# Kernel optimization log

Measured on AMD Instinct MI355X. Metric: run time of the kernel, lower is better.

The kernel has to match this reference:

```python
import jax, jax.numpy as jnp
import numpy as np

N = 50000      # nodes
E = 800000     # edges (avg degree 16)
G = 128        # graphs in batch
IN = 128       # in_channels
H = 128        # hidden_dim
C = 10         # num_classes


def setup_inputs() -> dict:
    key = jax.random.key(0)
    ks = jax.random.split(key, 8)
    x = jax.random.normal(ks[0], (N, IN), dtype=jnp.float32)
    edge_index = jax.random.randint(ks[1], (2, E), 0, N)
    edge_attr = jax.random.uniform(ks[2], (E,), dtype=jnp.float32)
    batch = jnp.sort(jax.random.randint(ks[3], (N,), 0, G))
    def glorot(k, fan_in, fan_out):
        return jax.random.normal(k, (fan_in, fan_out), dtype=jnp.float32) / np.float32(np.sqrt(fan_in))
    return {
        "x": x,
        "edge_index": edge_index,
        "edge_attr": edge_attr,
        "batch": batch,
        "W1": glorot(ks[4], IN, H), "b1": jnp.zeros((H,), jnp.float32),
        "W2": glorot(ks[5], H, H), "b2": jnp.zeros((H,), jnp.float32),
        "W3": glorot(ks[6], H, C), "b3": jnp.zeros((C,), jnp.float32),
    }


def gcn_conv(x, src, dst, ew, W, b, n):
    # symmetric GCN normalization (self-loops already appended, weight 1)
    deg = jax.ops.segment_sum(ew, dst, num_segments=n)            # [N]
    dinv = jnp.where(deg > 0, jax.lax.rsqrt(deg), 0.0)
    norm = dinv[src] * ew * dinv[dst]                             # [E+N]
    h = x @ W                                                     # [N, out]
    agg = jax.ops.segment_sum(h[src] * norm[:, None], dst, num_segments=n)
    return agg + b


def reference(x, edge_index, edge_attr, batch, W1, b1, W2, b2, W3, b3):
    n = x.shape[0]
    loop = jnp.arange(n)
    src = jnp.concatenate([edge_index[0], loop])
    dst = jnp.concatenate([edge_index[1], loop])
    ew = jnp.concatenate([edge_attr, jnp.ones((n,), edge_attr.dtype)])
    h = jax.nn.relu(gcn_conv(x, src, dst, ew, W1, b1, n))   # dropout is identity in eval
    h = jax.nn.relu(gcn_conv(h, src, dst, ew, W2, b2, n))
    h = gcn_conv(h, src, dst, ew, W3, b3, n)                 # [N, C]
    # global mean pool over graphs
    sums = jax.ops.segment_sum(h, batch, num_segments=G)     # [G, C]
    cnt = jax.ops.segment_sum(jnp.ones((n,), h.dtype), batch, num_segments=G)
    pooled = sums / jnp.maximum(cnt, 1.0)[:, None]
    return jax.nn.log_softmax(pooled, axis=1)
```

## Files before the change

### kernel.cpp

```cpp
#include <hip/hip_runtime.h>

#define NN 50000
#define NE 800000
#define NG 128
#define DIM 128
#define CO 10
#define CAP 64

typedef unsigned long long ull;
typedef unsigned short ushort;

static __device__ __forceinline__ ushort f2bf(float f) {
    unsigned int u = __float_as_uint(f);
    unsigned int r = (u + 0x7FFF + ((u >> 16) & 1)) >> 16;
    return (ushort)r;
}

__global__ void k_ell(const int* __restrict__ src, const int* __restrict__ dst,
                      const float* __restrict__ ew, int* __restrict__ cnt,
                      ull* __restrict__ ell) {
    int e = blockIdx.x * blockDim.x + threadIdx.x;
    if (e >= NE) return;
    int d = dst[e], s = src[e];
    int slot = atomicAdd(&cnt[d], 1);
    if (slot < CAP) {
        ull rec = ((ull)__float_as_uint(ew[e]) << 32) | (unsigned int)s;
        ell[(size_t)d * CAP + slot] = rec;
    }
}

__global__ __launch_bounds__(256) void k_deg(const int* __restrict__ cnt,
                                             const ull* __restrict__ ell,
                                             float* __restrict__ dinv) {
    int node = blockIdx.x * 4 + (threadIdx.x >> 6);
    int lane = threadIdx.x & 63;
    if (node >= NN) return;
    int n = cnt[node];
    float w = 0.0f;
    if (lane < n) w = __uint_as_float((unsigned int)(ell[(size_t)node * CAP + lane] >> 32));
#pragma unroll
    for (int off = 32; off; off >>= 1) w += __shfl_down(w, off);
    if (lane == 0) dinv[node] = rsqrtf(1.0f + w);
}

__global__ __launch_bounds__(256) void k_scale(const int* __restrict__ cnt,
                                               ull* __restrict__ ell,
                                               const float* __restrict__ dinv) {
    int node = blockIdx.x * 4 + (threadIdx.x >> 6);
    int lane = threadIdx.x & 63;
    if (node >= NN) return;
    int n = cnt[node];
    if (lane >= n) return;
    size_t idx = (size_t)node * CAP + lane;
    ull rec = ell[idx];
    int s = (int)(unsigned int)(rec & 0xffffffffu);
    float ew = __uint_as_float((unsigned int)(rec >> 32));
    float v = dinv[node] * ew * dinv[s];
    ell[idx] = ((ull)__float_as_uint(v) << 32) | (unsigned int)s;
}

__global__ __launch_bounds__(256) void k_gemm128(const float* __restrict__ A,
                                                 const float* __restrict__ W,
                                                 ushort* __restrict__ C, int M) {
    __shared__ float As[64][33];
    __shared__ float Bs[32][132];
    int tid = threadIdx.x;
    int block_row = blockIdx.x * 64;
    int tx = tid & 15;
    int ty = tid >> 4;
    int r0 = ty * 4;
    int c1 = tx * 4, c2 = 64 + tx * 4;
    float acc[4][8];
#pragma unroll
    for (int i = 0; i < 4; i++)
#pragma unroll
        for (int j = 0; j < 8; j++) acc[i][j] = 0.0f;

    for (int k0 = 0; k0 < 128; k0 += 32) {
#pragma unroll
        for (int l = 0; l < 2; l++) {
            int idx = tid + l * 256;
            int ar = idx >> 3;
            int ac = (idx & 7) * 4;
            int grow = block_row + ar;
            if (grow >= M) grow = M - 1;
            float4 v = *(const float4*)&A[(size_t)grow * 128 + k0 + ac];
            As[ar][ac + 0] = v.x; As[ar][ac + 1] = v.y;
            As[ar][ac + 2] = v.z; As[ar][ac + 3] = v.w;
        }
#pragma unroll
        for (int l = 0; l < 4; l++) {
            int idx = tid + l * 256;
            int br = idx >> 5;
            int bc = (idx & 31) * 4;
            float4 v = *(const float4*)&W[(size_t)(k0 + br) * 128 + bc];
            *(float4*)&Bs[br][bc] = v;
        }
        __syncthreads();
#pragma unroll
        for (int kk = 0; kk < 32; kk++) {
            float a0 = As[r0 + 0][kk];
            float a1 = As[r0 + 1][kk];
            float a2 = As[r0 + 2][kk];
            float a3 = As[r0 + 3][kk];
            float4 bl = *(float4*)&Bs[kk][c1];
            float4 bh = *(float4*)&Bs[kk][c2];
            acc[0][0] += a0 * bl.x; acc[0][1] += a0 * bl.y; acc[0][2] += a0 * bl.z; acc[0][3] += a0 * bl.w;
            acc[0][4] += a0 * bh.x; acc[0][5] += a0 * bh.y; acc[0][6] += a0 * bh.z; acc[0][7] += a0 * bh.w;
            acc[1][0] += a1 * bl.x; acc[1][1] += a1 * bl.y; acc[1][2] += a1 * bl.z; acc[1][3] += a1 * bl.w;
            acc[1][4] += a1 * bh.x; acc[1][5] += a1 * bh.y; acc[1][6] += a1 * bh.z; acc[1][7] += a1 * bh.w;
            acc[2][0] += a2 * bl.x; acc[2][1] += a2 * bl.y; acc[2][2] += a2 * bl.z; acc[2][3] += a2 * bl.w;
            acc[2][4] += a2 * bh.x; acc[2][5] += a2 * bh.y; acc[2][6] += a2 * bh.z; acc[2][7] += a2 * bh.w;
            acc[3][0] += a3 * bl.x; acc[3][1] += a3 * bl.y; acc[3][2] += a3 * bl.z; acc[3][3] += a3 * bl.w;
            acc[3][4] += a3 * bh.x; acc[3][5] += a3 * bh.y; acc[3][6] += a3 * bh.z; acc[3][7] += a3 * bh.w;
        }
        __syncthreads();
    }
#pragma unroll
    for (int i = 0; i < 4; i++) {
        int grow = block_row + r0 + i;
        if (grow < M) {
            ushort4 u1, u2;
            u1.x = f2bf(acc[i][0]); u1.y = f2bf(acc[i][1]); u1.z = f2bf(acc[i][2]); u1.w = f2bf(acc[i][3]);
            u2.x = f2bf(acc[i][4]); u2.y = f2bf(acc[i][5]); u2.z = f2bf(acc[i][6]); u2.w = f2bf(acc[i][7]);
            *(ushort4*)&C[(size_t)grow * 128 + c1] = u1;
            *(ushort4*)&C[(size_t)grow * 128 + c2] = u2;
        }
    }
}

__global__ __launch_bounds__(256) void k_gemm10(const float* __restrict__ A,
                                                const float* __restrict__ W3,
                                                float* __restrict__ C3, int M) {
    __shared__ float Ws[1280];
    int tid = threadIdx.x;
    for (int i = tid; i < 1280; i += 256) Ws[i] = W3[i];
    __syncthreads();
    int col = tid & 15;
    int rloc = tid >> 4;
    int row = blockIdx.x * 16 + rloc;
    if (row >= M || col >= 10) return;
    const float* a = &A[(size_t)row * 128];
    float acc = 0.0f;
#pragma unroll
    for (int k = 0; k < 128; k += 4) {
        float4 av = *(const float4*)&a[k];
        acc += av.x * Ws[(k + 0) * 10 + col];
        acc += av.y * Ws[(k + 1) * 10 + col];
        acc += av.z * Ws[(k + 2) * 10 + col];
        acc += av.w * Ws[(k + 3) * 10 + col];
    }
    C3[(size_t)row * 10 + col] = acc;
}

__global__ __launch_bounds__(256) void k_gather128(const int* __restrict__ cnt,
                                                   const ull* __restrict__ ell,
                                                   const float* __restrict__ dinv,
                                                   const ushort* __restrict__ h,
                                                   const float* __restrict__ b,
                                                   float* __restrict__ outp,
                                                   int do_relu) {
    int node = blockIdx.x * 4 + (threadIdx.x >> 6);
    int lane = threadIdx.x & 63;
    if (node >= NN) return;
    int n = cnt[node];
    float di = dinv[node];
    unsigned int hp = *(const unsigned int*)&h[(size_t)node * 128 + lane * 2];
    float ax = di * di * __uint_as_float(hp << 16);
    float ay = di * di * __uint_as_float(hp & 0xffff0000u);
    ull rec = ell[(size_t)node * CAP + lane];
    int ce = (int)(unsigned int)(rec & 0xffffffffu);
    float we = __uint_as_float((unsigned int)(rec >> 32));
    int j = 0;
    for (; j + 3 < n; j += 4) {
        int s0 = __shfl(ce, j + 0), s1 = __shfl(ce, j + 1);
        int s2 = __shfl(ce, j + 2), s3 = __shfl(ce, j + 3);
        float w0 = __shfl(we, j + 0), w1 = __shfl(we, j + 1);
        float w2 = __shfl(we, j + 2), w3 = __shfl(we, j + 3);
        unsigned int p0 = *(const unsigned int*)&h[(size_t)s0 * 128 + lane * 2];
        unsigned int p1 = *(const unsigned int*)&h[(size_t)s1 * 128 + lane * 2];
        unsigned int p2 = *(const unsigned int*)&h[(size_t)s2 * 128 + lane * 2];
        unsigned int p3 = *(const unsigned int*)&h[(size_t)s3 * 128 + lane * 2];
        ax += w0 * __uint_as_float(p0 << 16) + w1 * __uint_as_float(p1 << 16)
            + w2 * __uint_as_float(p2 << 16) + w3 * __uint_as_float(p3 << 16);
        ay += w0 * __uint_as_float(p0 & 0xffff0000u) + w1 * __uint_as_float(p1 & 0xffff0000u)
            + w2 * __uint_as_float(p2 & 0xffff0000u) + w3 * __uint_as_float(p3 & 0xffff0000u);
    }
    for (; j < n; j++) {
        int s0 = __shfl(ce, j);
        float w0 = __shfl(we, j);
        unsigned int p0 = *(const unsigned int*)&h[(size_t)s0 * 128 + lane * 2];
        ax += w0 * __uint_as_float(p0 << 16);
        ay += w0 * __uint_as_float(p0 & 0xffff0000u);
    }
    ax += b[lane * 2 + 0];
    ay += b[lane * 2 + 1];
    if (do_relu) { ax = fmaxf(ax, 0.0f); ay = fmaxf(ay, 0.0f); }
    float2 o; o.x = ax; o.y = ay;
    *(float2*)&outp[(size_t)node * 128 + lane * 2] = o;
}

__global__ __launch_bounds__(256) void k_edge_pool(const int* __restrict__ src,
                                                   const int* __restrict__ dst,
                                                   const float* __restrict__ ew,
                                                   const float* __restrict__ dinv,
                                                   const float* __restrict__ z,
                                                   const int* __restrict__ batch,
                                                   float* __restrict__ sums,
                                                   float* __restrict__ cntf) {
    __shared__ float ls[NG * CO + NG];
    for (int i = threadIdx.x; i < NG * CO + NG; i += 256) ls[i] = 0.0f;
    __syncthreads();
    const int total = NE + NN;
    for (int idx = blockIdx.x * 256 + threadIdx.x; idx < total; idx += gridDim.x * 256) {
        int s, g; float w;
        if (idx < NE) {
            s = src[idx];
            int d = dst[idx];
            w = dinv[s] * ew[idx] * dinv[d];
            g = batch[d];
        } else {
            int i = idx - NE;
            s = i;
            float di = dinv[i];
            w = di * di;
            g = batch[i];
            atomicAdd(&ls[NG * CO + g], 1.0f);
        }
        const float* zp = &z[(size_t)s * 10];
        float* lp = &ls[g * 10];
#pragma unroll
        for (int f = 0; f < 10; f++) atomicAdd(&lp[f], w * zp[f]);
    }
    __syncthreads();
    for (int i = threadIdx.x; i < NG * CO + NG; i += 256) {
        float v = ls[i];
        if (v != 0.0f) {
            if (i < NG * CO) atomicAdd(&sums[i], v);
            else atomicAdd(&cntf[i - NG * CO], v);
        }
    }
}

__global__ void k_logsoftmax(const float* __restrict__ sums,
                             const float* __restrict__ cntf,
                             const float* __restrict__ b3,
                             float* __restrict__ out) {
    int g = threadIdx.x;
    if (g >= NG) return;
    float c = fmaxf(cntf[g], 1.0f);
    float p[10];
    float m = -1e30f;
#pragma unroll
    for (int f = 0; f < 10; f++) {
        p[f] = sums[g * 10 + f] / c + b3[f];
        m = fmaxf(m, p[f]);
    }
    float s = 0.0f;
#pragma unroll
    for (int f = 0; f < 10; f++) s += __expf(p[f] - m);
    float lse = m + __logf(s);
#pragma unroll
    for (int f = 0; f < 10; f++) out[g * 10 + f] = p[f] - lse;
}

extern "C" void kernel_launch(void* const* d_in, const int* in_sizes, int n_in,
                              void* d_out, int out_size, void* d_ws, size_t ws_size,
                              hipStream_t stream) {
    const float* x     = (const float*)d_in[0];
    const int*   ei    = (const int*)d_in[1];
    const float* ea    = (const float*)d_in[2];
    const int*   batch = (const int*)d_in[3];
    const float* W1    = (const float*)d_in[4];
    const float* b1    = (const float*)d_in[5];
    const float* W2    = (const float*)d_in[6];
    const float* b2    = (const float*)d_in[7];
    const float* W3    = (const float*)d_in[8];
    const float* b3    = (const float*)d_in[9];
    float* out = (float*)d_out;
    float* ws  = (float*)d_ws;

    const int* esrc = ei;
    const int* edst = ei + NE;

    float*  bufA = ws;
    ushort* hb   = (ushort*)(ws + 6400000);
    float*  z    = ws + 9600000;
    float*  dinv = ws + 10100000;
    float*  sums = ws + 10150000;
    float*  cntf = ws + 10151280;
    int*    cnt  = (int*)(ws + 10160000);
    ull*    ell  = (ull*)(ws + 10210000);

    hipMemsetAsync(cnt, 0, NN * sizeof(int), stream);
    k_ell<<<(NE + 255) / 256, 256, 0, stream>>>(esrc, edst, ea, cnt, ell);
    k_deg<<<(NN + 3) / 4, 256, 0, stream>>>(cnt, ell, dinv);
    k_scale<<<(NN + 3) / 4, 256, 0, stream>>>(cnt, ell, dinv);

    k_gemm128<<<(NN + 63) / 64, 256, 0, stream>>>(x, W1, hb, NN);
    k_gather128<<<(NN + 3) / 4, 256, 0, stream>>>(cnt, ell, dinv, hb, b1, bufA, 1);

    k_gemm128<<<(NN + 63) / 64, 256, 0, stream>>>(bufA, W2, hb, NN);
    k_gather128<<<(NN + 3) / 4, 256, 0, stream>>>(cnt, ell, dinv, hb, b2, bufA, 1);

    k_gemm10<<<(NN + 15) / 16, 256, 0, stream>>>(bufA, W3, z, NN);
    hipMemsetAsync(sums, 0, (NG * CO + NG) * sizeof(float), stream);
    k_edge_pool<<<512, 256, 0, stream>>>(esrc, edst, ea, dinv, z, batch, sums, cntf);

    k_logsoftmax<<<1, 128, 0, stream>>>(sums, cntf, b3, out);
}
```

Measured before the change: 345.8 us.

## Pool layer-3 output via ELL node gather with deterministic per-block partials

Replaces the edge-parallel final pooling kernel, which did per-edge shared-memory atomics for 10 features, with a node-per-wave pass. Each wave reads the prebuilt ELL rows, reduces the 10 features with shuffles, and does one atomic per graph slot per node. Per-block partials are written to workspace and reduced by a new final kernel that also applies log-softmax, removing the memset and global atomics. The cost is a partial buffer of 512 blocks x 1408 floats that must be read back in a second pass.

```diff
diff --git a/kernel.cpp b/kernel.cpp
--- a/kernel.cpp
+++ b/kernel.cpp
@@ -6,6 +6,7 @@
 #define DIM 128
 #define CO 10
 #define CAP 64
+#define NB 512
 
 typedef unsigned long long ull;
 typedef unsigned short ushort;
@@ -200,68 +201,83 @@
     *(float2*)&outp[(size_t)node * 128 + lane * 2] = o;
 }
 
-__global__ __launch_bounds__(256) void k_edge_pool(const int* __restrict__ src,
-                                                   const int* __restrict__ dst,
-                                                   const float* __restrict__ ew,
+__global__ __launch_bounds__(256) void k_pool_node(const int* __restrict__ cnt,
+                                                   const ull* __restrict__ ell,
                                                    const float* __restrict__ dinv,
                                                    const float* __restrict__ z,
                                                    const int* __restrict__ batch,
-                                                   float* __restrict__ sums,
-                                                   float* __restrict__ cntf) {
+                                                   float* __restrict__ partial) {
     __shared__ float ls[NG * CO + NG];
     for (int i = threadIdx.x; i < NG * CO + NG; i += 256) ls[i] = 0.0f;
     __syncthreads();
-    const int total = NE + NN;
-    for (int idx = blockIdx.x * 256 + threadIdx.x; idx < total; idx += gridDim.x * 256) {
-        int s, g; float w;
-        if (idx < NE) {
-            s = src[idx];
-            int d = dst[idx];
-            w = dinv[s] * ew[idx] * dinv[d];
-            g = batch[d];
-        } else {
-            int i = idx - NE;
-            s = i;
-            float di = dinv[i];
+    int lane = threadIdx.x & 63;
+    int gwave = blockIdx.x * 4 + (threadIdx.x >> 6);
+    for (int node = gwave; node < NN; node += NB * 4) {
+        int n = cnt[node];
+        float w = 0.0f; int s = 0;
+        if (lane < n) {
+            ull rec = ell[(size_t)node * CAP + lane];
+            s = (int)(unsigned int)(rec & 0xffffffffu);
+            w = __uint_as_float((unsigned int)(rec >> 32));
+        } else if (lane == n) {
+            s = node;
+            float di = dinv[node];
             w = di * di;
-            g = batch[i];
+        }
+        const float* zp = &z[(size_t)s * 10];
+        float v[10];
+#pragma unroll
+        for (int f = 0; f < 10; f++) v[f] = w * zp[f];
+#pragma unroll
+        for (int off = 32; off; off >>= 1) {
+#pragma unroll
+            for (int f = 0; f < 10; f++) v[f] += __shfl_down(v[f], off);
+        }
+        if (lane == 0) {
+            int g = batch[node];
+            float* lp = &ls[g * 10];
+#pragma unroll
+            for (int f = 0; f < 10; f++) atomicAdd(&lp[f], v[f]);
             atomicAdd(&ls[NG * CO + g], 1.0f);
         }
-        const float* zp = &z[(size_t)s * 10];
-        float* lp = &ls[g * 10];
-#pragma unroll
-        for (int f = 0; f < 10; f++) atomicAdd(&lp[f], w * zp[f]);
     }
     __syncthreads();
-    for (int i = threadIdx.x; i < NG * CO + NG; i += 256) {
-        float v = ls[i];
-        if (v != 0.0f) {
-            if (i < NG * CO) atomicAdd(&sums[i], v);
-            else atomicAdd(&cntf[i - NG * CO], v);
-        }
-    }
-}
-
-__global__ void k_logsoftmax(const float* __restrict__ sums,
-                             const float* __restrict__ cntf,
+    float* pb = &partial[(size_t)blockIdx.x * (NG * CO + NG)];
+    for (int i = threadIdx.x; i < NG * CO + NG; i += 256) pb[i] = ls[i];
+}
+
+__global__ void k_pool_final(const float* __restrict__ partial,
                              const float* __restrict__ b3,
                              float* __restrict__ out) {
-    int g = threadIdx.x;
-    if (g >= NG) return;
-    float c = fmaxf(cntf[g], 1.0f);
-    float p[10];
-    float m = -1e30f;
-#pragma unroll
-    for (int f = 0; f < 10; f++) {
-        p[f] = sums[g * 10 + f] / c + b3[f];
-        m = fmaxf(m, p[f]);
-    }
-    float s = 0.0f;
-#pragma unroll
-    for (int f = 0; f < 10; f++) s += __expf(p[f] - m);
-    float lse = m + __logf(s);
-#pragma unroll
-    for (int f = 0; f < 10; f++) out[g * 10 + f] = p[f] - lse;
+    int g = blockIdx.x;
+    int lane = threadIdx.x;
+    float v[10]; float c = 0.0f;
+#pragma unroll
+    for (int f = 0; f < 10; f++) v[f] = 0.0f;
+    for (int b = lane; b < NB; b += 64) {
+        const float* pb = &partial[(size_t)b * (NG * CO + NG)];
+#pragma unroll
+        for (int f = 0; f < 10; f++) v[f] += pb[g * 10 + f];
+        c += pb[NG * CO + g];
+    }
+#pragma unroll
+    for (int off = 32; off; off >>= 1) {
+#pragma unroll
+        for (int f = 0; f < 10; f++) v[f] += __shfl_down(v[f], off);
+        c += __shfl_down(c, off);
+    }
+    if (lane == 0) {
+        c = fmaxf(c, 1.0f);
+        float p[10], m = -1e30f;
+#pragma unroll
+        for (int f = 0; f < 10; f++) { p[f] = v[f] / c + b3[f]; m = fmaxf(m, p[f]); }
+        float ssum = 0.0f;
+#pragma unroll
+        for (int f = 0; f < 10; f++) ssum += __expf(p[f] - m);
+        float lse = m + __logf(ssum);
+#pragma unroll
+        for (int f = 0; f < 10; f++) out[g * 10 + f] = p[f] - lse;
+    }
 }
 
 extern "C" void kernel_launch(void* const* d_in, const int* in_sizes, int n_in,
@@ -283,14 +299,13 @@
     const int* esrc = ei;
     const int* edst = ei + NE;
 
-    float*  bufA = ws;
-    ushort* hb   = (ushort*)(ws + 6400000);
-    float*  z    = ws + 9600000;
-    float*  dinv = ws + 10100000;
-    float*  sums = ws + 10150000;
-    float*  cntf = ws + 10151280;
-    int*    cnt  = (int*)(ws + 10160000);
-    ull*    ell  = (ull*)(ws + 10210000);
+    float*  bufA    = ws;
+    ushort* hb      = (ushort*)(ws + 6400000);
+    float*  z       = ws + 9600000;
+    float*  dinv    = ws + 10100000;
+    int*    cnt     = (int*)(ws + 10160000);
+    ull*    ell     = (ull*)(ws + 10210000);
+    float*  partial = ws + 16610000;
 
     hipMemsetAsync(cnt, 0, NN * sizeof(int), stream);
     k_ell<<<(NE + 255) / 256, 256, 0, stream>>>(esrc, edst, ea, cnt, ell);
@@ -304,8 +319,6 @@
     k_gather128<<<(NN + 3) / 4, 256, 0, stream>>>(cnt, ell, dinv, hb, b2, bufA, 1);
 
     k_gemm10<<<(NN + 15) / 16, 256, 0, stream>>>(bufA, W3, z, NN);
-    hipMemsetAsync(sums, 0, (NG * CO + NG) * sizeof(float), stream);
-    k_edge_pool<<<512, 256, 0, stream>>>(esrc, edst, ea, dinv, z, batch, sums, cntf);
-
-    k_logsoftmax<<<1, 128, 0, stream>>>(sums, cntf, b3, out);
-}
+    k_pool_node<<<NB, 256, 0, stream>>>(cnt, ell, dinv, z, batch, partial);
+    k_pool_final<<<NG, 64, 0, stream>>>(partial, b3, out);
+}
```

New measurement: 346.0 us. About the same (+0.1%).
